# Kernel tuning notes

Measured on AMD Instinct MI355X. Metric: run time of the kernel, lower is better.

## Reference

```python
import jax, jax.numpy as jnp
import numpy as np

B, CIN, COUT, H, W, K, G = 2, 256, 256, 128, 128, 3, 4
PAD = (K - 1) // 2


def setup_inputs() -> dict:
    key = jax.random.key(0)
    k1, k2, k3, k4 = jax.random.split(key, 4)
    x = jax.random.normal(k1, (B, CIN, H, W), dtype=jnp.float32)
    # conv_offset: 1x1 conv, out channels = G*2*K*K. (Zero-init in the module; use
    # small random weights so offsets are non-trivial for correctness testing.)
    w_offset = jax.random.normal(k2, (G * 2 * K * K, CIN), dtype=jnp.float32) * 0.01
    b_offset = jax.random.normal(k3, (G * 2 * K * K,), dtype=jnp.float32) * 0.5
    # DeformConv weight (bias=False in mmcv DeformConv)
    w_deform = jax.random.normal(k4, (COUT, CIN, K, K), dtype=jnp.float32) * (1.0 / np.sqrt(CIN * K * K))
    return {"x": x, "w_offset": w_offset, "b_offset": b_offset, "w_deform": w_deform}


def _bilinear_gather(img, y, x):
    """img: [B,G,Cg,H,W]; y,x: [B,G,H,W] float sample coords -> [B,G,Cg,H,W].
    Zero padding outside the image (mmcv DCN bilinear semantics)."""
    b, g, cg, h, w = img.shape
    imgf = img.reshape(b, g, cg, h * w)
    y0 = jnp.floor(y)
    x0 = jnp.floor(x)
    out = jnp.zeros((b, g, cg, h * w), img.dtype)
    for yy, xx in ((y0, x0), (y0, x0 + 1.0), (y0 + 1.0, x0), (y0 + 1.0, x0 + 1.0)):
        wgt = (1.0 - jnp.abs(y - yy)) * (1.0 - jnp.abs(x - xx))
        valid = (yy >= 0) & (yy < h) & (xx >= 0) & (xx < w)
        wgt = jnp.where(valid, wgt, 0.0)
        yi = jnp.clip(yy, 0, h - 1).astype(jnp.int32)
        xi = jnp.clip(xx, 0, w - 1).astype(jnp.int32)
        idx = (yi * w + xi).reshape(b, g, 1, h * w)
        vals = jnp.take_along_axis(imgf, jnp.broadcast_to(idx, (b, g, cg, h * w)), axis=3)
        out = out + wgt.reshape(b, g, 1, h * w) * vals
    return out.reshape(b, g, cg, h, w)


def reference(x, w_offset, b_offset, w_deform):
    b, cin, h, w = x.shape
    cout, _, k, _ = w_deform.shape
    pad = (k - 1) // 2
    # 1x1 offset conv
    offset = jnp.einsum('bchw,oc->bohw', x, w_offset) + b_offset[None, :, None, None]
    g = offset.shape[1] // (2 * k * k)
    off = offset.reshape(b, g, k * k, 2, h, w)  # (dy, dx) per kernel tap, mmcv layout
    xg = x.reshape(b, g, cin // g, h, w)
    hh = jnp.arange(h, dtype=x.dtype)[:, None]
    ww = jnp.arange(w, dtype=x.dtype)[None, :]
    out = jnp.zeros((b, cout, h, w), x.dtype)
    for i in range(k):
        for j in range(k):
            t = i * k + j
            ys = hh - pad + i + off[:, :, t, 0]  # [B,G,H,W]
            xs = ww - pad + j + off[:, :, t, 1]
            samp = _bilinear_gather(xg, ys, xs).reshape(b, cin, h, w)
            out = out + jnp.einsum('bchw,oc->bohw', samp, w_deform[:, :, i, j])
    return jax.nn.relu(out)
```

## Files before the change

kernel.cpp:

```cpp
#include <hip/hip_runtime.h>
#include <stdint.h>

#define HW    16384
#define CIN   256
#define COUT  256
#define Hh    128
#define Ww    128
#define OFFC  72

typedef __attribute__((ext_vector_type(4))) float    f32x4;
typedef __attribute__((ext_vector_type(2))) _Float16 f16x2;
typedef __attribute__((ext_vector_type(8))) _Float16 f16x8;
typedef unsigned short u16;
typedef unsigned int   u32;

__device__ __forceinline__ u16 f2h(float f) { return __builtin_bit_cast(u16, (_Float16)f); }
__device__ __forceinline__ u32 pk2(float f) { u32 h = f2h(f); return h | (h << 16); }
__device__ __forceinline__ f16x2 bch(u32 u) { return __builtin_bit_cast(f16x2, u); }

__global__ __launch_bounds__(256) void kprep(const float* __restrict__ x, const float* __restrict__ wd,
                                             const float* __restrict__ wo, u16* __restrict__ xt,
                                             u16* __restrict__ wfrag, u16* __restrict__ wfrag2) {
  __shared__ float smem[9216];
  int blk = blockIdx.x;
  if (blk < 2048) {
    int bg = blk >> 8;
    int p0 = (blk & 255) << 6;
    const float* src = x + (size_t)bg * 64 * HW + p0;
    #pragma unroll
    for (int r = 0; r < 16; ++r) {
      int idx = threadIdx.x + 256 * r;
      int c = idx >> 6, px = idx & 63;
      smem[c * 65 + px] = src[(size_t)c * HW + px];
    }
    __syncthreads();
    int px = threadIdx.x >> 2, seg = threadIdx.x & 3;
    u32 w[8];
    #pragma unroll
    for (int k = 0; k < 8; ++k) {
      float lo = smem[(seg * 16 + 2 * k) * 65 + px];
      float hi = smem[(seg * 16 + 2 * k + 1) * 65 + px];
      w[k] = (u32)f2h(lo) | ((u32)f2h(hi) << 16);
    }
    u16* dst = xt + ((size_t)bg * HW + p0 + px) * 64 + seg * 16;
    *(uint4*)dst       = make_uint4(w[0], w[1], w[2], w[3]);
    *(uint4*)(dst + 8) = make_uint4(w[4], w[5], w[6], w[7]);
  } else if (blk < 2112) {
    int bb = blk - 2048;
    int nt = bb & 15;
    int g  = bb >> 4;
    const float* src = wd + (size_t)(nt * 16) * 2304 + (size_t)g * 64 * 9;
    #pragma unroll
    for (int r = 0; r < 36; ++r) {
      int idx = threadIdx.x + 256 * r;
      int cl  = idx / 576;
      int rem = idx - cl * 576;
      smem[cl * 576 + rem] = src[(size_t)cl * 2304 + rem];
    }
    __syncthreads();
    #pragma unroll
    for (int r = 0; r < 36; ++r) {
      int o    = threadIdx.x + 256 * r;
      int j    = o & 7;
      int lane = (o >> 3) & 63;
      int kcl  = o >> 9;
      int t = kcl >> 1, half = kcl & 1;
      int n = lane & 15, q = lane >> 4;
      int cg = half * 32 + q * 8 + j;
      float v = smem[n * 576 + cg * 9 + t];
      int kc = (g * 9 + t) * 2 + half;
      wfrag[(size_t)((kc * 16 + nt) * 64 + lane) * 8 + j] = f2h(v);
    }
  } else {
    int e = (blk - 2112) * 256 + threadIdx.x;
    int j = e & 7;
    int lane = (e >> 3) & 63;
    int idx = e >> 9;
    int kc = idx / 5, nt = idx - 5 * kc;
    int n16 = lane & 15, q = lane >> 4;
    int oc = nt * 16 + n16;
    int c  = kc * 32 + q * 8 + j;
    float v = (oc < OFFC) ? wo[(size_t)oc * CIN + c] : 0.f;
    wfrag2[e] = f2h(v);
  }
}

__device__ __forceinline__ void mkpre(float yy, float xx, int* ob, u32* wp) {
  float y0f = floorf(yy), x0f = floorf(xx);
  float fy = yy - y0f, fx = xx - x0f;
  int y0 = (int)y0f, x0 = (int)x0f;
  int y1 = y0 + 1, x1 = x0 + 1;
  float vy0 = (y0 >= 0 && y0 < Hh) ? 1.f : 0.f;
  float vy1 = (y1 >= 0 && y1 < Hh) ? 1.f : 0.f;
  float vx0 = (x0 >= 0 && x0 < Ww) ? 1.f : 0.f;
  float vx1 = (x1 >= 0 && x1 < Ww) ? 1.f : 0.f;
  wp[0] = pk2((1.f - fy) * (1.f - fx) * vy0 * vx0);
  wp[1] = pk2((1.f - fy) * fx * vy0 * vx1);
  wp[2] = pk2(fy * (1.f - fx) * vy1 * vx0);
  wp[3] = pk2(fy * fx * vy1 * vx1);
  int cy0 = min(max(y0, 0), Hh - 1), cy1 = min(max(y1, 0), Hh - 1);
  int cx0 = min(max(x0, 0), Ww - 1), cx1 = min(max(x1, 0), Ww - 1);
  ob[0] = (cy0 * Ww + cx0) << 7;
  ob[1] = (cy0 * Ww + cx1) << 7;
  ob[2] = (cy1 * Ww + cx0) << 7;
  ob[3] = (cy1 * Ww + cx1) << 7;
}

__device__ __forceinline__ uint4 bil16(uint4 a, uint4 b, uint4 c, uint4 d, const u32* wp) {
  f16x2 W0 = bch(wp[0]), W1 = bch(wp[1]), W2 = bch(wp[2]), W3 = bch(wp[3]);
  uint4 r;
  { f16x2 s = bch(a.x) * W0 + bch(b.x) * W1 + bch(c.x) * W2 + bch(d.x) * W3; r.x = __builtin_bit_cast(u32, s); }
  { f16x2 s = bch(a.y) * W0 + bch(b.y) * W1 + bch(c.y) * W2 + bch(d.y) * W3; r.y = __builtin_bit_cast(u32, s); }
  { f16x2 s = bch(a.z) * W0 + bch(b.z) * W1 + bch(c.z) * W2 + bch(d.z) * W3; r.z = __builtin_bit_cast(u32, s); }
  { f16x2 s = bch(a.w) * W0 + bch(b.w) * W1 + bch(c.w) * W2 + bch(d.w) * W3; r.w = __builtin_bit_cast(u32, s); }
  return r;
}

__global__ __launch_bounds__(256, 2) void k2(const u16* __restrict__ xt, const u16* __restrict__ wfrag2,
                                             const float* __restrict__ bo, const u16* __restrict__ wfrag,
                                             float* __restrict__ out) {
  __shared__ u16   astage[3 * 4096];
  __shared__ float offl[36 * 128];
  int tid = threadIdx.x;
  int lane = tid & 63, n16 = lane & 15, q = (tid >> 4) & 3;
  int wv = tid >> 6;
  int b  = blockIdx.x >> 8;
  int p0 = (blockIdx.x & 255) << 6;
  int h  = p0 >> 7, w0 = p0 & 127;
  const char* xtb = (const char*)xt + (size_t)b * 4 * HW * 128;

  {
    f32x4 oacc[5];
    #pragma unroll
    for (int nt = 0; nt < 5; ++nt) {
      int oc = nt * 16 + n16;
      float bv = (oc < OFFC) ? bo[oc] : 0.f;
      oacc[nt] = (f32x4){bv, bv, bv, bv};
    }
    #pragma unroll
    for (int kc = 0; kc < 8; ++kc) {
      int g = kc >> 1;
      f16x8 af = __builtin_bit_cast(f16x8, *(const uint4*)(xtb +
          ((size_t)(g * HW + p0 + wv * 16 + n16)) * 128 + (kc & 1) * 64 + q * 16));
      #pragma unroll
      for (int nt = 0; nt < 5; ++nt) {
        f16x8 bf = __builtin_bit_cast(f16x8, *(const uint4*)(wfrag2 + (size_t)(((kc * 5 + nt) << 6) + lane) * 8));
        oacc[nt] = __builtin_amdgcn_mfma_f32_16x16x32_f16(af, bf, oacc[nt], 0, 0, 0);
      }
    }
    #pragma unroll
    for (int nt = 0; nt < 5; ++nt) {
      int oc = nt * 16 + n16;
      if (oc < OFFC) {
        int gt = oc >> 1, comp = oc & 1;
        #pragma unroll
        for (int r = 0; r < 4; ++r)
          offl[(gt * 64 + wv * 16 + q * 4 + r) * 2 + comp] = oacc[nt][r];
      }
    }
  }
  __syncthreads();

  float fh = (float)h;
  float fx = (float)(w0 + wv * 16 + n16);
  int chb = q * 16;
  int pxl = wv * 16 + n16;

  f32x4 acc[4][4];
  #pragma unroll
  for (int mt = 0; mt < 4; ++mt)
    #pragma unroll
    for (int j = 0; j < 4; ++j) acc[mt][j] = (f32x4){0.f, 0.f, 0.f, 0.f};

  auto issue = [&](int gt, uint4* d, u32* wp) {
    float2 o = *(const float2*)&offl[(gt * 64 + pxl) * 2];
    int g = (gt * 57) >> 9;
    int t = gt - g * 9;
    int i = (t * 683) >> 11;
    int j = t - i * 3;
    int ob[4];
    mkpre(fh + (float)(i - 1) + o.x, fx + (float)(j - 1) + o.y, ob, wp);
    const char* xg = xtb + (size_t)g * HW * 128;
    #pragma unroll
    for (int c = 0; c < 4; ++c) {
      d[c]     = *(const uint4*)(xg + ob[c] + chb);
      d[4 + c] = *(const uint4*)(xg + ob[c] + chb + 64);
    }
  };
  auto produce = [&](int slot, const uint4* d, const u32* wp) {
    *(uint4*)&astage[(slot * 8 + wv * 2 + 0) * 512 + lane * 8] = bil16(d[0], d[1], d[2], d[3], wp);
    *(uint4*)&astage[(slot * 8 + wv * 2 + 1) * 512 + lane * 8] = bil16(d[4], d[5], d[6], d[7], wp);
  };
  auto loadB = [&](int gt, uint4* bf) {
    const u16* wb = wfrag + (size_t)gt * 16384 + (size_t)(wv * 4) * 512 + (size_t)lane * 8;
    #pragma unroll
    for (int hh = 0; hh < 2; ++hh)
      #pragma unroll
      for (int j = 0; j < 4; ++j)
        bf[hh * 4 + j] = *(const uint4*)(wb + (size_t)(hh * 16 + j) * 512);
  };
  auto consume = [&](int slot, const uint4* bf) {
    #pragma unroll
    for (int hh = 0; hh < 2; ++hh) {
      f16x8 af[4];
      #pragma unroll
      for (int mt = 0; mt < 4; ++mt)
        af[mt] = __builtin_bit_cast(f16x8,
            *(const uint4*)&astage[(slot * 8 + mt * 2 + hh) * 512 + lane * 8]);
      #pragma unroll
      for (int mt = 0; mt < 4; ++mt)
        #pragma unroll
        for (int j = 0; j < 4; ++j)
          acc[mt][j] = __builtin_amdgcn_mfma_f32_16x16x32_f16(
              af[mt], __builtin_bit_cast(f16x8, bf[hh * 4 + j]), acc[mt][j], 0, 0, 0);
    }
  };

  uint4 dA[8], dB[8];
  u32   wpA[4], wpB[4];
  uint4 bfA[8], bfB[8];
  issue(0, dA, wpA);
  issue(1, dB, wpB);
  produce(0, dA, wpA);
  loadB(0, bfA);
  __syncthreads();

  #pragma unroll 1
  for (int gt = 0; gt < 36; gt += 2) {
    produce((gt + 1) % 3, dB, wpB);
    if (gt + 2 < 36) issue(gt + 2, dA, wpA);
    loadB(gt + 1, bfB);
    __syncthreads();
    consume(gt % 3, bfA);
    if (gt + 2 < 36) {
      produce((gt + 2) % 3, dA, wpA);
      if (gt + 3 < 36) issue(gt + 3, dB, wpB);
      loadB(gt + 2, bfA);
      __syncthreads();
    }
    consume((gt + 1) % 3, bfB);
  }

  float* op = out + (size_t)b * COUT * HW + p0;
  #pragma unroll
  for (int mt = 0; mt < 4; ++mt)
    #pragma unroll
    for (int j = 0; j < 4; ++j) {
      f32x4 v = acc[mt][j];
      #pragma unroll
      for (int r = 0; r < 4; ++r) v[r] = fmaxf(v[r], 0.f);
      int cout = wv * 64 + j * 16 + n16;
      *(f32x4*)(op + (size_t)cout * HW + mt * 16 + q * 4) = v;
    }
}

extern "C" void kernel_launch(void* const* d_in, const int* in_sizes, int n_in,
                              void* d_out, int out_size, void* d_ws, size_t ws_size,
                              hipStream_t stream) {
  const float* x  = (const float*)d_in[0];
  const float* wo = (const float*)d_in[1];
  const float* bo = (const float*)d_in[2];
  const float* wd = (const float*)d_in[3];
  float* out = (float*)d_out;

  u16* xtp    = (u16*)d_ws;
  u16* wfrag  = (u16*)((char*)d_ws + 16777216);
  u16* wfrag2 = (u16*)((char*)d_ws + 16777216 + 1179648);

  kprep<<<2192, 256, 0, stream>>>(x, wd, wo, xtp, wfrag, wfrag2);
  k2   <<<512,  256, 0, stream>>>(xtp, wfrag2, bo, wfrag, out);
}
```

Baseline: 198.3 us.

## Split deform conv into producer and consumer wavefronts with double-buffered staging

The main kernel now launches 512 threads per block. Four wavefronts do the bilinear gather and interpolation, and four others run the MFMA GEMM and the offset conv, synchronised through a double-buffered LDS stage. The aim is to overlap the gather latency with matrix math using warp specialization instead of interleaving both in one wave. The prep kernel also switches to vectorized float4 loads for the x transpose and splits weight fragment packing across twice as many blocks with half the shared memory. The risks are more barriers per tap, with a sync every step, and higher register pressure from the launch bounds of 512 threads and 4 blocks.

```diff
diff --git a/kernel.cpp b/kernel.cpp
--- a/kernel.cpp
+++ b/kernel.cpp
@@ -21,17 +21,21 @@
 __global__ __launch_bounds__(256) void kprep(const float* __restrict__ x, const float* __restrict__ wd,
                                              const float* __restrict__ wo, u16* __restrict__ xt,
                                              u16* __restrict__ wfrag, u16* __restrict__ wfrag2) {
-  __shared__ float smem[9216];
+  __shared__ float smem[4608];
   int blk = blockIdx.x;
   if (blk < 2048) {
     int bg = blk >> 8;
     int p0 = (blk & 255) << 6;
     const float* src = x + (size_t)bg * 64 * HW + p0;
     #pragma unroll
-    for (int r = 0; r < 16; ++r) {
-      int idx = threadIdx.x + 256 * r;
+    for (int r = 0; r < 4; ++r) {
+      int idx = (threadIdx.x + 256 * r) * 4;
       int c = idx >> 6, px = idx & 63;
-      smem[c * 65 + px] = src[(size_t)c * HW + px];
+      f32x4 v = *(const f32x4*)(src + (size_t)c * HW + px);
+      smem[c * 65 + px + 0] = v[0];
+      smem[c * 65 + px + 1] = v[1];
+      smem[c * 65 + px + 2] = v[2];
+      smem[c * 65 + px + 3] = v[3];
     }
     __syncthreads();
     int px = threadIdx.x >> 2, seg = threadIdx.x & 3;
@@ -45,34 +49,36 @@
     u16* dst = xt + ((size_t)bg * HW + p0 + px) * 64 + seg * 16;
     *(uint4*)dst       = make_uint4(w[0], w[1], w[2], w[3]);
     *(uint4*)(dst + 8) = make_uint4(w[4], w[5], w[6], w[7]);
-  } else if (blk < 2112) {
+  } else if (blk < 2176) {
     int bb = blk - 2048;
-    int nt = bb & 15;
-    int g  = bb >> 4;
-    const float* src = wd + (size_t)(nt * 16) * 2304 + (size_t)g * 64 * 9;
-    #pragma unroll
-    for (int r = 0; r < 36; ++r) {
+    int nh = bb & 31;
+    int g  = bb >> 5;
+    const float* src = wd + (size_t)(nh * 8) * 2304 + (size_t)g * 64 * 9;
+    #pragma unroll
+    for (int r = 0; r < 18; ++r) {
       int idx = threadIdx.x + 256 * r;
       int cl  = idx / 576;
       int rem = idx - cl * 576;
       smem[cl * 576 + rem] = src[(size_t)cl * 2304 + rem];
     }
     __syncthreads();
-    #pragma unroll
-    for (int r = 0; r < 36; ++r) {
-      int o    = threadIdx.x + 256 * r;
-      int j    = o & 7;
-      int lane = (o >> 3) & 63;
-      int kcl  = o >> 9;
+    int nt = nh >> 1, nb = (nh & 1) * 8;
+    #pragma unroll
+    for (int r = 0; r < 18; ++r) {
+      int o  = threadIdx.x + 256 * r;
+      int j  = o & 7;
+      int n8 = (o >> 3) & 7;
+      int q  = (o >> 6) & 3;
+      int kcl = o >> 8;
       int t = kcl >> 1, half = kcl & 1;
-      int n = lane & 15, q = lane >> 4;
       int cg = half * 32 + q * 8 + j;
-      float v = smem[n * 576 + cg * 9 + t];
+      float v = smem[n8 * 576 + cg * 9 + t];
       int kc = (g * 9 + t) * 2 + half;
-      wfrag[(size_t)((kc * 16 + nt) * 64 + lane) * 8 + j] = f2h(v);
+      int lane = q * 16 + nb + n8;
+      wfrag[((size_t)(kc * 16 + nt) * 64 + lane) * 8 + j] = f2h(v);
     }
   } else {
-    int e = (blk - 2112) * 256 + threadIdx.x;
+    int e = (blk - 2176) * 256 + threadIdx.x;
     int j = e & 7;
     int lane = (e >> 3) & 63;
     int idx = e >> 9;
@@ -106,30 +112,40 @@
   ob[3] = (cy1 * Ww + cx1) << 7;
 }
 
-__device__ __forceinline__ uint4 bil16(uint4 a, uint4 b, uint4 c, uint4 d, const u32* wp) {
+__device__ __forceinline__ uint4 bil16(const uint4* v, const u32* wp) {
   f16x2 W0 = bch(wp[0]), W1 = bch(wp[1]), W2 = bch(wp[2]), W3 = bch(wp[3]);
   uint4 r;
-  { f16x2 s = bch(a.x) * W0 + bch(b.x) * W1 + bch(c.x) * W2 + bch(d.x) * W3; r.x = __builtin_bit_cast(u32, s); }
-  { f16x2 s = bch(a.y) * W0 + bch(b.y) * W1 + bch(c.y) * W2 + bch(d.y) * W3; r.y = __builtin_bit_cast(u32, s); }
-  { f16x2 s = bch(a.z) * W0 + bch(b.z) * W1 + bch(c.z) * W2 + bch(d.z) * W3; r.z = __builtin_bit_cast(u32, s); }
-  { f16x2 s = bch(a.w) * W0 + bch(b.w) * W1 + bch(c.w) * W2 + bch(d.w) * W3; r.w = __builtin_bit_cast(u32, s); }
+  { f16x2 s = bch(v[0].x) * W0 + bch(v[1].x) * W1 + bch(v[2].x) * W2 + bch(v[3].x) * W3; r.x = __builtin_bit_cast(u32, s); }
+  { f16x2 s = bch(v[0].y) * W0 + bch(v[1].y) * W1 + bch(v[2].y) * W2 + bch(v[3].y) * W3; r.y = __builtin_bit_cast(u32, s); }
+  { f16x2 s = bch(v[0].z) * W0 + bch(v[1].z) * W1 + bch(v[2].z) * W2 + bch(v[3].z) * W3; r.z = __builtin_bit_cast(u32, s); }
+  { f16x2 s = bch(v[0].w) * W0 + bch(v[1].w) * W1 + bch(v[2].w) * W2 + bch(v[3].w) * W3; r.w = __builtin_bit_cast(u32, s); }
   return r;
 }
 
-__global__ __launch_bounds__(256, 2) void k2(const u16* __restrict__ xt, const u16* __restrict__ wfrag2,
+__global__ __launch_bounds__(512, 4) void k2(const u16* __restrict__ xt, const u16* __restrict__ wfrag2,
                                              const float* __restrict__ bo, const u16* __restrict__ wfrag,
                                              float* __restrict__ out) {
-  __shared__ u16   astage[3 * 4096];
-  __shared__ float offl[36 * 128];
-  int tid = threadIdx.x;
+  __shared__ u16   astage[2 * 8 * 512];
+  __shared__ float offl[36 * 64 * 2];
+  int tid  = threadIdx.x;
   int lane = tid & 63, n16 = lane & 15, q = (tid >> 4) & 3;
-  int wv = tid >> 6;
+  int wv   = tid >> 6;
+  bool prod = wv < 4;
+  int  sw   = wv & 3;
   int b  = blockIdx.x >> 8;
   int p0 = (blockIdx.x & 255) << 6;
   int h  = p0 >> 7, w0 = p0 & 127;
   const char* xtb = (const char*)xt + (size_t)b * 4 * HW * 128;
-
-  {
+  float fh  = (float)h;
+  float fxp = (float)(w0 + sw * 16 + n16);
+  int   chb = q * 16;
+
+  f32x4 acc[4][4];
+  uint4 bf[8];
+  uint4 d[2][8];
+  u32   wp[2][4];
+
+  if (!prod) {
     f32x4 oacc[5];
     #pragma unroll
     for (int nt = 0; nt < 5; ++nt) {
@@ -141,11 +157,11 @@
     for (int kc = 0; kc < 8; ++kc) {
       int g = kc >> 1;
       f16x8 af = __builtin_bit_cast(f16x8, *(const uint4*)(xtb +
-          ((size_t)(g * HW + p0 + wv * 16 + n16)) * 128 + (kc & 1) * 64 + q * 16));
+          ((size_t)(g * HW + p0 + sw * 16 + n16)) * 128 + (kc & 1) * 64 + chb));
       #pragma unroll
       for (int nt = 0; nt < 5; ++nt) {
-        f16x8 bf = __builtin_bit_cast(f16x8, *(const uint4*)(wfrag2 + (size_t)(((kc * 5 + nt) << 6) + lane) * 8));
-        oacc[nt] = __builtin_amdgcn_mfma_f32_16x16x32_f16(af, bf, oacc[nt], 0, 0, 0);
+        f16x8 bfo = __builtin_bit_cast(f16x8, *(const uint4*)(wfrag2 + (size_t)(((kc * 5 + nt) << 6) + lane) * 8));
+        oacc[nt] = __builtin_amdgcn_mfma_f32_16x16x32_f16(af, bfo, oacc[nt], 0, 0, 0);
       }
     }
     #pragma unroll
@@ -155,103 +171,97 @@
         int gt = oc >> 1, comp = oc & 1;
         #pragma unroll
         for (int r = 0; r < 4; ++r)
-          offl[(gt * 64 + wv * 16 + q * 4 + r) * 2 + comp] = oacc[nt][r];
-      }
-    }
+          offl[(gt * 64 + sw * 16 + q * 4 + r) * 2 + comp] = oacc[nt][r];
+      }
+    }
+    #pragma unroll
+    for (int mt = 0; mt < 4; ++mt)
+      #pragma unroll
+      for (int j = 0; j < 4; ++j) acc[mt][j] = (f32x4){0.f, 0.f, 0.f, 0.f};
+    #pragma unroll
+    for (int hh = 0; hh < 2; ++hh)
+      #pragma unroll
+      for (int j = 0; j < 4; ++j)
+        bf[hh * 4 + j] = *(const uint4*)(wfrag + ((size_t)((hh * 16 + sw * 4 + j)) * 64 + lane) * 8);
   }
   __syncthreads();
 
-  float fh = (float)h;
-  float fx = (float)(w0 + wv * 16 + n16);
-  int chb = q * 16;
-  int pxl = wv * 16 + n16;
-
-  f32x4 acc[4][4];
-  #pragma unroll
-  for (int mt = 0; mt < 4; ++mt)
-    #pragma unroll
-    for (int j = 0; j < 4; ++j) acc[mt][j] = (f32x4){0.f, 0.f, 0.f, 0.f};
-
-  auto issue = [&](int gt, uint4* d, u32* wp) {
-    float2 o = *(const float2*)&offl[(gt * 64 + pxl) * 2];
+  auto issue = [&](int gt, uint4* dd, u32* wpp) {
+    float2 o = *(const float2*)&offl[(gt * 64 + sw * 16 + n16) * 2];
     int g = (gt * 57) >> 9;
     int t = gt - g * 9;
     int i = (t * 683) >> 11;
     int j = t - i * 3;
     int ob[4];
-    mkpre(fh + (float)(i - 1) + o.x, fx + (float)(j - 1) + o.y, ob, wp);
+    mkpre(fh + (float)(i - 1) + o.x, fxp + (float)(j - 1) + o.y, ob, wpp);
     const char* xg = xtb + (size_t)g * HW * 128;
     #pragma unroll
     for (int c = 0; c < 4; ++c) {
-      d[c]     = *(const uint4*)(xg + ob[c] + chb);
-      d[4 + c] = *(const uint4*)(xg + ob[c] + chb + 64);
+      dd[c]     = *(const uint4*)(xg + ob[c] + chb);
+      dd[4 + c] = *(const uint4*)(xg + ob[c] + chb + 64);
     }
   };
-  auto produce = [&](int slot, const uint4* d, const u32* wp) {
-    *(uint4*)&astage[(slot * 8 + wv * 2 + 0) * 512 + lane * 8] = bil16(d[0], d[1], d[2], d[3], wp);
-    *(uint4*)&astage[(slot * 8 + wv * 2 + 1) * 512 + lane * 8] = bil16(d[4], d[5], d[6], d[7], wp);
+  auto produce = [&](int slot, const uint4* dd, const u32* wpp) {
+    *(uint4*)&astage[(slot * 8 + sw * 2 + 0) * 512 + lane * 8] = bil16(dd,     wpp);
+    *(uint4*)&astage[(slot * 8 + sw * 2 + 1) * 512 + lane * 8] = bil16(dd + 4, wpp);
   };
-  auto loadB = [&](int gt, uint4* bf) {
-    const u16* wb = wfrag + (size_t)gt * 16384 + (size_t)(wv * 4) * 512 + (size_t)lane * 8;
-    #pragma unroll
-    for (int hh = 0; hh < 2; ++hh)
-      #pragma unroll
-      for (int j = 0; j < 4; ++j)
-        bf[hh * 4 + j] = *(const uint4*)(wb + (size_t)(hh * 16 + j) * 512);
-  };
-  auto consume = [&](int slot, const uint4* bf) {
-    #pragma unroll
-    for (int hh = 0; hh < 2; ++hh) {
-      f16x8 af[4];
-      #pragma unroll
-      for (int mt = 0; mt < 4; ++mt)
-        af[mt] = __builtin_bit_cast(f16x8,
-            *(const uint4*)&astage[(slot * 8 + mt * 2 + hh) * 512 + lane * 8]);
-      #pragma unroll
-      for (int mt = 0; mt < 4; ++mt)
-        #pragma unroll
-        for (int j = 0; j < 4; ++j)
-          acc[mt][j] = __builtin_amdgcn_mfma_f32_16x16x32_f16(
-              af[mt], __builtin_bit_cast(f16x8, bf[hh * 4 + j]), acc[mt][j], 0, 0, 0);
-    }
-  };
-
-  uint4 dA[8], dB[8];
-  u32   wpA[4], wpB[4];
-  uint4 bfA[8], bfB[8];
-  issue(0, dA, wpA);
-  issue(1, dB, wpB);
-  produce(0, dA, wpA);
-  loadB(0, bfA);
+
+  if (prod) {
+    issue(0, d[0], wp[0]);
+    issue(1, d[1], wp[1]);
+    produce(0, d[0], wp[0]);
+  }
   __syncthreads();
 
   #pragma unroll 1
-  for (int gt = 0; gt < 36; gt += 2) {
-    produce((gt + 1) % 3, dB, wpB);
-    if (gt + 2 < 36) issue(gt + 2, dA, wpA);
-    loadB(gt + 1, bfB);
+  for (int gt = 0; gt < 36; ++gt) {
+    if (prod) {
+      if (gt < 35) {
+        int s = (gt + 1) & 1;
+        produce(s, d[s], wp[s]);
+        if (gt + 2 < 36) issue(gt + 2, d[gt & 1], wp[gt & 1]);
+      }
+    } else {
+      int slot = gt & 1;
+      #pragma unroll
+      for (int hh = 0; hh < 2; ++hh) {
+        f16x8 af[4];
+        #pragma unroll
+        for (int mt = 0; mt < 4; ++mt)
+          af[mt] = __builtin_bit_cast(f16x8,
+              *(const uint4*)&astage[(slot * 8 + mt * 2 + hh) * 512 + lane * 8]);
+        #pragma unroll
+        for (int mt = 0; mt < 4; ++mt)
+          #pragma unroll
+          for (int j = 0; j < 4; ++j)
+            acc[mt][j] = __builtin_amdgcn_mfma_f32_16x16x32_f16(
+                af[mt], __builtin_bit_cast(f16x8, bf[hh * 4 + j]), acc[mt][j], 0, 0, 0);
+      }
+      if (gt < 35) {
+        const u16* wb = wfrag + (size_t)(2 * (gt + 1) * 16 + sw * 4) * 512 + (size_t)lane * 8;
+        #pragma unroll
+        for (int hh = 0; hh < 2; ++hh)
+          #pragma unroll
+          for (int j = 0; j < 4; ++j)
+            bf[hh * 4 + j] = *(const uint4*)(wb + (size_t)(hh * 16 + j) * 512);
+      }
+    }
     __syncthreads();
-    consume(gt % 3, bfA);
-    if (gt + 2 < 36) {
-      produce((gt + 2) % 3, dA, wpA);
-      if (gt + 3 < 36) issue(gt + 3, dB, wpB);
-      loadB(gt + 2, bfA);
-      __syncthreads();
-    }
-    consume((gt + 1) % 3, bfB);
-  }
-
-  float* op = out + (size_t)b * COUT * HW + p0;
-  #pragma unroll
-  for (int mt = 0; mt < 4; ++mt)
-    #pragma unroll
-    for (int j = 0; j < 4; ++j) {
-      f32x4 v = acc[mt][j];
-      #pragma unroll
-      for (int r = 0; r < 4; ++r) v[r] = fmaxf(v[r], 0.f);
-      int cout = wv * 64 + j * 16 + n16;
-      *(f32x4*)(op + (size_t)cout * HW + mt * 16 + q * 4) = v;
-    }
+  }
+
+  if (!prod) {
+    float* op = out + (size_t)b * COUT * HW + p0;
+    #pragma unroll
+    for (int mt = 0; mt < 4; ++mt)
+      #pragma unroll
+      for (int j = 0; j < 4; ++j) {
+        f32x4 v = acc[mt][j];
+        #pragma unroll
+        for (int r = 0; r < 4; ++r) v[r] = fmaxf(v[r], 0.f);
+        int cout = sw * 64 + j * 16 + n16;
+        *(f32x4*)(op + (size_t)cout * HW + mt * 16 + q * 4) = v;
+      }
+  }
 }
 
 extern "C" void kernel_launch(void* const* d_in, const int* in_sizes, int n_in,
@@ -267,6 +277,6 @@
   u16* wfrag  = (u16*)((char*)d_ws + 16777216);
   u16* wfrag2 = (u16*)((char*)d_ws + 16777216 + 1179648);
 
-  kprep<<<2192, 256, 0, stream>>>(x, wd, wo, xtp, wfrag, wfrag2);
-  k2   <<<512,  256, 0, stream>>>(xtp, wfrag2, bo, wfrag, out);
-}
+  kprep<<<2256, 256, 0, stream>>>(x, wd, wo, xtp, wfrag, wfrag2);
+  k2   <<<512,  512, 0, stream>>>(xtp, wfrag2, bo, wfrag, out);
+}
```

New measurement: 336.0 us. 1.69x slower.
